# Optimization experiments

Hardware: AMD Instinct MI355X
Metric: run time of the kernel (lower is better)

Reference implementation:

```python
import jax, jax.numpy as jnp
import numpy as np

N, E, D, ED, SH = 100000, 1600000, 64, 16, 9

# Real spherical harmonics l=0,1,2, 'integral' normalization (e3nn default),
# applied to unit direction vectors. Coefficients: 1/(2*sqrt(pi)), sqrt(3/4pi), etc.

def _sh(d):
    x, y, z = d[:, 0], d[:, 1], d[:, 2]
    return jnp.stack([
        jnp.full_like(x, 0.28209479177387814),          # l=0
        0.4886025119029199 * y,                          # l=1, m=-1
        0.4886025119029199 * z,                          # l=1, m=0
        0.4886025119029199 * x,                          # l=1, m=1
        1.0925484305920792 * x * y,                      # l=2, m=-2
        1.0925484305920792 * y * z,                      # l=2, m=-1
        0.31539156525252005 * (3.0 * z * z - 1.0),       # l=2, m=0
        1.0925484305920792 * x * z,                      # l=2, m=1
        0.5462742152960396 * (x * x - y * y),            # l=2, m=2
    ], axis=1)


def _mlp(h, W1, b1, W2, b2):  # Linear -> SiLU -> Linear
    return jax.nn.silu(h @ W1 + b1) @ W2 + b2


def setup_inputs() -> dict:
    key = jax.random.key(0)
    ks = jax.random.split(key, 16)
    def rn(k, shape, scale=0.05):
        return jax.random.normal(k, shape, dtype=jnp.float32) * scale
    return {
        "x": jax.random.normal(ks[0], (N, D), jnp.float32),
        "pos": jax.random.normal(ks[1], (N, 3), jnp.float32) * 3.0,
        "edge_attr": jax.random.normal(ks[2], (E, ED), jnp.float32),
        "row": jax.random.randint(ks[3], (E,), 0, N, dtype=jnp.int32),
        "col": jax.random.randint(ks[4], (E,), 0, N, dtype=jnp.int32),
        "node_W1": rn(ks[5], (D, D)), "node_b1": jnp.zeros((D,), jnp.float32),
        "node_W2": rn(ks[6], (D, D)), "node_b2": jnp.zeros((D,), jnp.float32),
        "edge_W1": rn(ks[7], (SH + ED, D)), "edge_b1": jnp.zeros((D,), jnp.float32),
        "edge_W2": rn(ks[8], (D, D)), "edge_b2": jnp.zeros((D,), jnp.float32),
        "out_W1": rn(ks[9], (2 * D, D)), "out_b1": jnp.zeros((D,), jnp.float32),
        "out_W2": rn(ks[10], (D, D)), "out_b2": jnp.zeros((D,), jnp.float32),
        "bn_gamma": jnp.ones((D,), jnp.float32), "bn_beta": jnp.zeros((D,), jnp.float32),
    }


def reference(x, pos, edge_attr, row, col,
              node_W1, node_b1, node_W2, node_b2,
              edge_W1, edge_b1, edge_W2, edge_b2,
              out_W1, out_b1, out_W2, out_b2,
              bn_gamma, bn_beta):
    # gather node positions per edge -> relative vectors
    rel = pos[row] - pos[col]                                    # [E,3]
    length = jnp.sqrt(jnp.sum(rel * rel, axis=1, keepdims=True) + 1e-12)
    d = rel / length
    d = d / (jnp.sqrt(jnp.sum(d * d, axis=1, keepdims=True)) + 1e-10)
    edge_sh = _sh(d)                                             # [E,9]
    edge_feat = jnp.concatenate([edge_sh, edge_attr], axis=1)    # [E,9+ED]
    x_t = _mlp(x, node_W1, node_b1, node_W2, node_b2)            # [N,D]
    e_w = _mlp(edge_feat, edge_W1, edge_b1, edge_W2, edge_b2)    # [E,D]
    msg = x_t[row] * e_w                                         # message = x_j * edge_attr
    # scatter-mean onto target nodes (edge_index[1] == col)
    s = jax.ops.segment_sum(msg, col, num_segments=N)            # [N,D]
    cnt = jax.ops.segment_sum(jnp.ones((E,), msg.dtype), col, num_segments=N)
    agg = s / jnp.maximum(cnt, 1.0)[:, None]
    h = jnp.concatenate([agg, x], axis=1)                        # [N,2D]
    h = _mlp(h, out_W1, out_b1, out_W2, out_b2)                  # [N,D]
    # BatchNorm over node dim (scalar irreps), training-mode batch stats
    mean = jnp.mean(h, axis=0)
    var = jnp.var(h, axis=0)
    return (h - mean) / jnp.sqrt(var + 1e-5) * bn_gamma + bn_beta
```

## Files before the change

### kernel.cpp

```cpp
#include <hip/hip_runtime.h>
#include <math.h>

#define DD 64
#define EDA 16

#define FR_E1 0
#define FR_E2 4
#define FR_N1 12
#define FR_N2 20
#define FR_O1 28
#define FR_O2 44
#define FR_TOT 52

#define PADH 72
#define PADF 68

typedef unsigned int u32;
typedef __attribute__((ext_vector_type(8))) short short8;
typedef __attribute__((ext_vector_type(4))) float f32x4;

static __device__ __forceinline__ float silu(float v) {
    return v / (1.0f + __expf(-v));
}
static __device__ __forceinline__ unsigned short f2bf(float f) {
    unsigned u = __float_as_uint(f);
    unsigned r = u + 0x7FFFu + ((u >> 16) & 1u);
    return (unsigned short)(r >> 16);
}
static __device__ __forceinline__ float bf2f(unsigned short u) {
    return __uint_as_float(((unsigned)u) << 16);
}
static __device__ __forceinline__ unsigned cvt_pk_bf16(float lo, float hi) {
    unsigned r;
    asm("v_cvt_pk_bf16_f32 %0, %1, %2" : "=v"(r) : "v"(lo), "v"(hi));
    return r;
}

__global__ __launch_bounds__(256) void k_pack_w(
    const float* __restrict__ eW1, const float* __restrict__ eW2,
    const float* __restrict__ nW1, const float* __restrict__ nW2,
    const float* __restrict__ oW1, const float* __restrict__ oW2,
    unsigned short* __restrict__ wpk)
{
    int t = threadIdx.x;
    int nt = t >> 6, l = t & 63;
    int kc = l >> 4, n0 = l & 15;

    #pragma unroll
    for (int j = 0; j < 8; ++j) {
        int k = kc*8 + j;
        int orig = (k < 16) ? (9 + k) : ((k < 25) ? (k - 16) : -1);
        float v = (orig >= 0) ? eW1[orig*DD + nt*16 + n0] : 0.0f;
        wpk[((size_t)((FR_E1 + nt)*64 + l))*8 + j] = f2bf(v);
    }
    #pragma unroll
    for (int s = 0; s < 2; ++s) {
        #pragma unroll
        for (int j = 0; j < 8; ++j) {
            int k = s*32 + kc*8 + j;
            wpk[((size_t)((FR_E2 + s*4 + nt)*64 + l))*8 + j] = f2bf(eW2[k*DD + nt*16 + n0]);
            wpk[((size_t)((FR_N1 + s*4 + nt)*64 + l))*8 + j] = f2bf(nW1[k*DD + nt*16 + n0]);
            wpk[((size_t)((FR_N2 + s*4 + nt)*64 + l))*8 + j] = f2bf(nW2[k*DD + nt*16 + n0]);
            wpk[((size_t)((FR_O2 + s*4 + nt)*64 + l))*8 + j] = f2bf(oW2[k*DD + nt*16 + n0]);
        }
    }
    #pragma unroll
    for (int s = 0; s < 4; ++s) {
        #pragma unroll
        for (int j = 0; j < 8; ++j) {
            int k = s*32 + kc*8 + j;
            wpk[((size_t)((FR_O1 + s*4 + nt)*64 + l))*8 + j] = f2bf(oW1[k*DD + nt*16 + n0]);
        }
    }
}

__global__ __launch_bounds__(256) void k_hist(
    const int* __restrict__ col, u32* __restrict__ cnt, int n_e)
{
    int g = blockIdx.x * 256 + threadIdx.x;
    int base = g * 4;
    if (base + 3 < n_e) {
        int4 c = ((const int4*)col)[g];
        atomicAdd(&cnt[c.x], 1u);
        atomicAdd(&cnt[c.y], 1u);
        atomicAdd(&cnt[c.z], 1u);
        atomicAdd(&cnt[c.w], 1u);
    } else {
        for (int e = base; e < n_e; ++e) atomicAdd(&cnt[col[e]], 1u);
    }
}

__global__ __launch_bounds__(256) void k_scan1(
    const u32* __restrict__ cnt, u32* __restrict__ bsum, int n)
{
    __shared__ u32 s[256];
    int i = blockIdx.x * 256 + threadIdx.x;
    s[threadIdx.x] = (i < n) ? cnt[i] : 0u;
    __syncthreads();
    for (int o = 128; o > 0; o >>= 1) {
        if (threadIdx.x < o) s[threadIdx.x] += s[threadIdx.x + o];
        __syncthreads();
    }
    if (threadIdx.x == 0) bsum[blockIdx.x] = s[0];
}

__global__ __launch_bounds__(512) void k_scan2(
    const u32* __restrict__ bsum, u32* __restrict__ boff, int nb)
{
    __shared__ u32 s[512];
    int t = threadIdx.x;
    u32 v = (t < nb) ? bsum[t] : 0u;
    s[t] = v;
    __syncthreads();
    for (int o = 1; o < 512; o <<= 1) {
        u32 a = (t >= o) ? s[t - o] : 0u;
        __syncthreads();
        s[t] += a;
        __syncthreads();
    }
    if (t < nb) boff[t] = s[t] - v;
}

__global__ __launch_bounds__(256) void k_scan3(
    const u32* __restrict__ cnt, const u32* __restrict__ boff,
    u32* __restrict__ wp, int n)
{
    __shared__ u32 s[256];
    int t = threadIdx.x;
    int i = blockIdx.x * 256 + t;
    u32 v = (i < n) ? cnt[i] : 0u;
    s[t] = v;
    __syncthreads();
    for (int o = 1; o < 256; o <<= 1) {
        u32 a = (t >= o) ? s[t - o] : 0u;
        __syncthreads();
        s[t] += a;
        __syncthreads();
    }
    if (i < n) wp[i] = boff[blockIdx.x] + s[t] - v;
}

__global__ __launch_bounds__(256) void k_scatter(
    const int* __restrict__ row, const int* __restrict__ col,
    u32* __restrict__ wp,
    int* __restrict__ esorted, int* __restrict__ rsorted, int* __restrict__ csorted,
    int n_e)
{
    int e = blockIdx.x * 256 + threadIdx.x;
    if (e >= n_e) return;
    int c = col[e];
    u32 p = atomicAdd(&wp[c], 1u);
    esorted[p] = e;
    rsorted[p] = row[e];
    csorted[p] = c;
}

__global__ __launch_bounds__(256, 2) void k_node_mfma(
    const float* __restrict__ x,
    const unsigned short* __restrict__ wpk,
    const float* __restrict__ b1, const float* __restrict__ b2,
    unsigned short* __restrict__ x_tb, int n)
{
    __shared__ __align__(16) unsigned short tile[4][16*PADH];
    const int tid  = threadIdx.x;
    const int wv   = tid >> 6;
    const int lane = tid & 63;
    const int kc   = lane >> 4;
    const int n0   = lane & 15;
    const int rbase = kc * 4;

    const short8* fb = (const short8*)wpk;
    short8 bw1[2][4], bw2[2][4];
    #pragma unroll
    for (int s = 0; s < 2; ++s)
        #pragma unroll
        for (int nt = 0; nt < 4; ++nt) {
            bw1[s][nt] = fb[(FR_N1 + s*4 + nt)*64 + lane];
            bw2[s][nt] = fb[(FR_N2 + s*4 + nt)*64 + lane];
        }
    float b1v[4], b2v[4];
    #pragma unroll
    for (int nt = 0; nt < 4; ++nt) { b1v[nt] = b1[nt*16 + n0]; b2v[nt] = b2[nt*16 + n0]; }

    const int base = blockIdx.x*64 + wv*16;
    int rc = min(base + n0, n - 1);
    const float* xr = x + (size_t)rc * DD;

    short8 a[2];
    #pragma unroll
    for (int m = 0; m < 2; ++m) {
        float4 u0 = *(const float4*)(xr + m*32 + kc*8);
        float4 u1 = *(const float4*)(xr + m*32 + kc*8 + 4);
        unsigned* au = (unsigned*)&a[m];
        au[0] = cvt_pk_bf16(u0.x, u0.y);
        au[1] = cvt_pk_bf16(u0.z, u0.w);
        au[2] = cvt_pk_bf16(u1.x, u1.y);
        au[3] = cvt_pk_bf16(u1.z, u1.w);
    }

    f32x4 zz = {0.f, 0.f, 0.f, 0.f};
    f32x4 hacc[4] = {zz, zz, zz, zz};
    #pragma unroll
    for (int m = 0; m < 2; ++m)
        #pragma unroll
        for (int nt = 0; nt < 4; ++nt)
            hacc[nt] = __builtin_amdgcn_mfma_f32_16x16x32_bf16(a[m], bw1[m][nt], hacc[nt], 0, 0, 0);

    #pragma unroll
    for (int nt = 0; nt < 4; ++nt)
        #pragma unroll
        for (int r = 0; r < 4; ++r)
            tile[wv][(rbase + r)*PADH + nt*16 + n0] = f2bf(silu(hacc[nt][r] + b1v[nt]));
    __syncthreads();

    short8 a2_0 = *(const short8*)&tile[wv][n0*PADH +  0 + kc*8];
    short8 a2_1 = *(const short8*)&tile[wv][n0*PADH + 32 + kc*8];
    f32x4 oacc[4];
    #pragma unroll
    for (int nt = 0; nt < 4; ++nt) {
        oacc[nt] = __builtin_amdgcn_mfma_f32_16x16x32_bf16(a2_0, bw2[0][nt], zz, 0, 0, 0);
        oacc[nt] = __builtin_amdgcn_mfma_f32_16x16x32_bf16(a2_1, bw2[1][nt], oacc[nt], 0, 0, 0);
    }
    __syncthreads();

    #pragma unroll
    for (int nt = 0; nt < 4; ++nt)
        #pragma unroll
        for (int r = 0; r < 4; ++r)
            tile[wv][(rbase + r)*PADH + nt*16 + n0] = f2bf(oacc[nt][r] + b2v[nt]);
    __syncthreads();

    int ei = lane >> 2, q = lane & 3;
    int er = base + ei;
    if (er < n) {
        uint4* dst = (uint4*)(x_tb + (size_t)er * DD);
        dst[q]     = *(const uint4*)&tile[wv][ei*PADH + q*8];
        dst[q + 4] = *(const uint4*)&tile[wv][ei*PADH + (q + 4)*8];
    }
}

__global__ __launch_bounds__(256) void k_edge_fused(
    const float* __restrict__ pos,
    const float* __restrict__ edge_attr,
    const int* __restrict__ esorted, const int* __restrict__ rsorted,
    const int* __restrict__ csorted,
    const unsigned short* __restrict__ x_tb,
    const unsigned short* __restrict__ wpk,
    const float* __restrict__ b1, const float* __restrict__ b2,
    float* __restrict__ agg, int n_e)
{
    __shared__ __align__(16) unsigned short hid_s[4][16*PADH];
    __shared__ __align__(16) float          msg_s[4][16*PADF];
    __shared__ __align__(16) unsigned short xls[4][16*DD];
    __shared__ int col_s[4][64];

    const int tid  = threadIdx.x;
    const int wv   = tid >> 6;
    const int lane = tid & 63;
    const int kc   = lane >> 4;
    const int n0   = lane & 15;
    const int rb   = kc * 4;

    const short8* fb = (const short8*)wpk;
    short8 bw1[4], bw2[2][4];
    #pragma unroll
    for (int nt = 0; nt < 4; ++nt) bw1[nt] = fb[(FR_E1 + nt)*64 + lane];
    #pragma unroll
    for (int s = 0; s < 2; ++s)
        #pragma unroll
        for (int nt = 0; nt < 4; ++nt) bw2[s][nt] = fb[(FR_E2 + s*4 + nt)*64 + lane];

    float b1v[4], b2v[4];
    #pragma unroll
    for (int nt = 0; nt < 4; ++nt) { b1v[nt] = b1[nt*16 + n0]; b2v[nt] = b2[nt*16 + n0]; }

    const int gbase = blockIdx.x*256 + wv*64;
    int g  = gbase + lane;
    int gc = min(g, n_e - 1);
    int eo = esorted[gc];
    int rw = rsorted[gc];
    int cl = csorted[gc];
    col_s[wv][lane] = cl;

    float ax = pos[3*rw+0] - pos[3*cl+0];
    float ay = pos[3*rw+1] - pos[3*cl+1];
    float az = pos[3*rw+2] - pos[3*cl+2];
    float len = sqrtf(fmaf(ax,ax, fmaf(ay,ay, az*az)) + 1e-12f);
    float dx = ax/len, dy = ay/len, dz = az/len;
    float n2 = sqrtf(fmaf(dx,dx, fmaf(dy,dy, dz*dz)));
    float inv = 1.0f/(n2 + 1e-10f);
    dx *= inv; dy *= inv; dz *= inv;

    float sh[9];
    sh[0] = 0.28209479177387814f;
    sh[1] = 0.4886025119029199f*dy;
    sh[2] = 0.4886025119029199f*dz;
    sh[3] = 0.4886025119029199f*dx;
    sh[4] = 1.0925484305920792f*dx*dy;
    sh[5] = 1.0925484305920792f*dy*dz;
    sh[6] = 0.31539156525252005f*(3.0f*dz*dz - 1.0f);
    sh[7] = 1.0925484305920792f*dx*dz;
    sh[8] = 0.5462742152960396f*(dx*dx - dy*dy);

    f32x4 zz = {0.f, 0.f, 0.f, 0.f};

    #pragma unroll 1
    for (int t = 0; t < 4; ++t) {
        {
            int lr = t*16 + (lane >> 2);
            int rv = __shfl(rw, lr);
            int ch = lane & 3;
            const uint4* src = (const uint4*)(x_tb + (size_t)rv * DD);
            uint4 v0 = src[ch*2], v1 = src[ch*2 + 1];
            uint4* d = (uint4*)&xls[wv][(lr - t*16)*DD];
            d[ch*2]     = v0;
            d[ch*2 + 1] = v1;
        }

        int le = t*16 + n0;
        float shv[8], sh8;
        #pragma unroll
        for (int j = 0; j < 8; ++j) shv[j] = __shfl(sh[j], le);
        sh8 = __shfl(sh[8], le);

        float fv[8];
        #pragma unroll
        for (int j = 0; j < 8; ++j) fv[j] = 0.0f;
        if (kc < 2) {
            int ea = __shfl(eo, le);
            const float4* ap = (const float4*)(edge_attr + (size_t)ea*EDA + kc*8);
            float4 a0 = ap[0], a1 = ap[1];
            fv[0]=a0.x; fv[1]=a0.y; fv[2]=a0.z; fv[3]=a0.w;
            fv[4]=a1.x; fv[5]=a1.y; fv[6]=a1.z; fv[7]=a1.w;
        } else if (kc == 2) {
            #pragma unroll
            for (int j = 0; j < 8; ++j) fv[j] = shv[j];
        } else {
            fv[0] = sh8;
        }

        short8 af;
        {
            unsigned* au = (unsigned*)&af;
            au[0] = cvt_pk_bf16(fv[0], fv[1]);
            au[1] = cvt_pk_bf16(fv[2], fv[3]);
            au[2] = cvt_pk_bf16(fv[4], fv[5]);
            au[3] = cvt_pk_bf16(fv[6], fv[7]);
        }

        f32x4 hacc[4];
        #pragma unroll
        for (int nt = 0; nt < 4; ++nt)
            hacc[nt] = __builtin_amdgcn_mfma_f32_16x16x32_bf16(af, bw1[nt], zz, 0, 0, 0);

        #pragma unroll
        for (int nt = 0; nt < 4; ++nt)
            #pragma unroll
            for (int r = 0; r < 4; ++r)
                hid_s[wv][(rb + r)*PADH + nt*16 + n0] = f2bf(silu(hacc[nt][r] + b1v[nt]));
        __syncthreads();

        short8 a2_0 = *(const short8*)&hid_s[wv][n0*PADH +  0 + kc*8];
        short8 a2_1 = *(const short8*)&hid_s[wv][n0*PADH + 32 + kc*8];
        f32x4 oacc[4];
        #pragma unroll
        for (int nt = 0; nt < 4; ++nt) {
            oacc[nt] = __builtin_amdgcn_mfma_f32_16x16x32_bf16(a2_0, bw2[0][nt], zz, 0, 0, 0);
            oacc[nt] = __builtin_amdgcn_mfma_f32_16x16x32_bf16(a2_1, bw2[1][nt], oacc[nt], 0, 0, 0);
        }

        #pragma unroll
        for (int r = 0; r < 4; ++r) {
            int lrow = rb + r;
            bool rv2 = (gbase + t*16 + lrow) < n_e;
            #pragma unroll
            for (int nt = 0; nt < 4; ++nt) {
                float xv = bf2f(xls[wv][lrow*DD + nt*16 + n0]);
                float m  = (oacc[nt][r] + b2v[nt]) * xv;
                msg_s[wv][lrow*PADF + nt*16 + n0] = rv2 ? m : 0.0f;
            }
        }
        __syncthreads();

        {
            const int* cs = &col_s[wv][t*16];
            float acc = 0.0f;
            #pragma unroll
            for (int r = 0; r < 16; ++r) {
                acc += msg_s[wv][r*PADF + lane];
                int cur = cs[r];
                bool flush = (r == 15) || (cs[r+1] != cur);
                if (flush) {
                    unsafeAtomicAdd(&agg[(size_t)cur*DD + lane], acc);
                    acc = 0.0f;
                }
            }
        }
        __syncthreads();
    }
}

__global__ __launch_bounds__(256, 2) void k_out_mfma(
    const float* __restrict__ agg, const u32* __restrict__ cnt,
    const float* __restrict__ x,
    const unsigned short* __restrict__ wpk,
    const float* __restrict__ b1, const float* __restrict__ b2,
    float* __restrict__ h, float* __restrict__ sums, int n)
{
    __shared__ __align__(16) unsigned short htile[4][16*PADH];
    __shared__ __align__(16) float otile[4][16*PADF];
    const int tid  = threadIdx.x;
    const int wv   = tid >> 6;
    const int lane = tid & 63;
    const int kc   = lane >> 4;
    const int n0   = lane & 15;
    const int rbase = kc * 4;

    const short8* fb = (const short8*)wpk;
    short8 bw1[4][4], bw2[2][4];
    #pragma unroll
    for (int s = 0; s < 4; ++s)
        #pragma unroll
        for (int nt = 0; nt < 4; ++nt) bw1[s][nt] = fb[(FR_O1 + s*4 + nt)*64 + lane];
    #pragma unroll
    for (int s = 0; s < 2; ++s)
        #pragma unroll
        for (int nt = 0; nt < 4; ++nt) bw2[s][nt] = fb[(FR_O2 + s*4 + nt)*64 + lane];

    float b1v[4], b2v[4];
    #pragma unroll
    for (int nt = 0; nt < 4; ++nt) { b1v[nt] = b1[nt*16 + n0]; b2v[nt] = b2[nt*16 + n0]; }

    const int base = blockIdx.x*64 + wv*16;
    int rc = min(base + n0, n - 1);
    const float* ar = agg + (size_t)rc * DD;
    const float* xr = x   + (size_t)rc * DD;
    float invc = 1.0f / fmaxf((float)cnt[rc], 1.0f);

    short8 a[4];
    #pragma unroll
    for (int m = 0; m < 4; ++m) {
        const float* src = (m < 2) ? (ar + m*32 + kc*8) : (xr + (m-2)*32 + kc*8);
        float4 u0 = *(const float4*)(src);
        float4 u1 = *(const float4*)(src + 4);
        if (m < 2) {
            u0.x*=invc; u0.y*=invc; u0.z*=invc; u0.w*=invc;
            u1.x*=invc; u1.y*=invc; u1.z*=invc; u1.w*=invc;
        }
        unsigned* au = (unsigned*)&a[m];
        au[0] = cvt_pk_bf16(u0.x, u0.y);
        au[1] = cvt_pk_bf16(u0.z, u0.w);
        au[2] = cvt_pk_bf16(u1.x, u1.y);
        au[3] = cvt_pk_bf16(u1.z, u1.w);
    }

    f32x4 zz = {0.f, 0.f, 0.f, 0.f};
    f32x4 hacc[4] = {zz, zz, zz, zz};
    #pragma unroll
    for (int m = 0; m < 4; ++m)
        #pragma unroll
        for (int nt = 0; nt < 4; ++nt)
            hacc[nt] = __builtin_amdgcn_mfma_f32_16x16x32_bf16(a[m], bw1[m][nt], hacc[nt], 0, 0, 0);

    #pragma unroll
    for (int nt = 0; nt < 4; ++nt)
        #pragma unroll
        for (int r = 0; r < 4; ++r)
            htile[wv][(rbase + r)*PADH + nt*16 + n0] = f2bf(silu(hacc[nt][r] + b1v[nt]));
    __syncthreads();

    short8 a2_0 = *(const short8*)&htile[wv][n0*PADH +  0 + kc*8];
    short8 a2_1 = *(const short8*)&htile[wv][n0*PADH + 32 + kc*8];
    f32x4 oacc[4];
    #pragma unroll
    for (int nt = 0; nt < 4; ++nt) {
        oacc[nt] = __builtin_amdgcn_mfma_f32_16x16x32_bf16(a2_0, bw2[0][nt], zz, 0, 0, 0);
        oacc[nt] = __builtin_amdgcn_mfma_f32_16x16x32_bf16(a2_1, bw2[1][nt], oacc[nt], 0, 0, 0);
    }

    #pragma unroll
    for (int nt = 0; nt < 4; ++nt)
        #pragma unroll
        for (int r = 0; r < 4; ++r)
            otile[wv][(rbase + r)*PADF + nt*16 + n0] = oacc[nt][r] + b2v[nt];
    __syncthreads();

    int ei = lane >> 2, q = lane & 3;
    int er = base + ei;
    if (er < n) {
        float4* dst = (float4*)(h + (size_t)er * DD);
        #pragma unroll
        for (int k = 0; k < 4; ++k)
            dst[q + 4*k] = *(const float4*)&otile[wv][ei*PADF + (q + 4*k)*4];
    }

    if (tid < 64) {
        int f = tid;
        float s = 0.f, qq = 0.f;
        #pragma unroll
        for (int w = 0; w < 4; ++w) {
            int base_w = blockIdx.x*64 + w*16;
            int nv = n - base_w;
            nv = nv < 0 ? 0 : (nv > 16 ? 16 : nv);
            for (int r = 0; r < nv; ++r) {
                float v = otile[w][r*PADF + f];
                s += v; qq = fmaf(v, v, qq);
            }
        }
        unsafeAtomicAdd(&sums[f], s);
        unsafeAtomicAdd(&sums[DD + f], qq);
    }
}

__global__ void k_bn_finalize(const float* __restrict__ sums,
                              const float* __restrict__ gamma, const float* __restrict__ beta,
                              float* __restrict__ ss, float inv_n)
{
    int j = threadIdx.x;
    float m = sums[j] * inv_n;
    float var = sums[DD+j] * inv_n - m*m;
    float sc = gamma[j] * rsqrtf(var + 1e-5f);
    ss[j] = sc;
    ss[DD+j] = beta[j] - m*sc;
}

__global__ __launch_bounds__(256) void k_bn_norm(
    float* __restrict__ h, const float* __restrict__ ss, int total4)
{
    int g = blockIdx.x*256 + threadIdx.x;
    if (g >= total4) return;
    int f0 = (g*4) & (DD-1);
    float4 v = ((const float4*)h)[g];
    v.x = fmaf(v.x, ss[f0+0], ss[DD+f0+0]);
    v.y = fmaf(v.y, ss[f0+1], ss[DD+f0+1]);
    v.z = fmaf(v.z, ss[f0+2], ss[DD+f0+2]);
    v.w = fmaf(v.w, ss[f0+3], ss[DD+f0+3]);
    ((float4*)h)[g] = v;
}

static inline size_t al16(size_t v) { return (v + 15) & ~(size_t)15; }

extern "C" void kernel_launch(void* const* d_in, const int* in_sizes, int n_in,
                              void* d_out, int out_size, void* d_ws, size_t ws_size,
                              hipStream_t stream)
{
    const float* x         = (const float*)d_in[0];
    const float* pos       = (const float*)d_in[1];
    const float* edge_attr = (const float*)d_in[2];
    const int*   row       = (const int*)d_in[3];
    const int*   col       = (const int*)d_in[4];
    const float* nW1 = (const float*)d_in[5];
    const float* nb1 = (const float*)d_in[6];
    const float* nW2 = (const float*)d_in[7];
    const float* nb2 = (const float*)d_in[8];
    const float* eW1 = (const float*)d_in[9];
    const float* eb1 = (const float*)d_in[10];
    const float* eW2 = (const float*)d_in[11];
    const float* eb2 = (const float*)d_in[12];
    const float* oW1 = (const float*)d_in[13];
    const float* ob1 = (const float*)d_in[14];
    const float* oW2 = (const float*)d_in[15];
    const float* ob2 = (const float*)d_in[16];
    const float* gamma = (const float*)d_in[17];
    const float* beta  = (const float*)d_in[18];

    const int N = in_sizes[0] / DD;
    const int E = in_sizes[3];
    const int NB = (N + 255) / 256;

    float* hout = (float*)d_out;
    char* ws = (char*)d_ws;

    size_t o_xtb  = 0;
    size_t o_cnt  = o_xtb  + (size_t)N*DD*2;
    size_t o_sums = o_cnt  + (size_t)N*4;
    size_t o_agg  = o_sums + 128*4;
    size_t o_ss   = o_agg  + (size_t)N*DD*4;
    size_t o_wp   = o_ss   + 128*4;
    size_t o_bsum = o_wp   + (size_t)N*4;
    size_t o_boff = al16(o_bsum + (size_t)NB*4);
    size_t o_wpk  = al16(o_boff + (size_t)NB*4);
    size_t o_eso  = al16(o_wpk + (size_t)FR_TOT*64*8*2);
    size_t o_rso  = o_eso + (size_t)E*4;
    size_t o_cso  = o_rso + (size_t)E*4;
    size_t need   = o_cso + (size_t)E*4;

    if (ws_size < need) return;

    unsigned short* x_tb = (unsigned short*)(ws + o_xtb);
    u32*   cnt  = (u32*)(ws + o_cnt);
    float* sums = (float*)(ws + o_sums);
    float* agg  = (float*)(ws + o_agg);
    float* ssb  = (float*)(ws + o_ss);
    u32*   wp   = (u32*)(ws + o_wp);
    u32*   bsum = (u32*)(ws + o_bsum);
    u32*   boff = (u32*)(ws + o_boff);
    unsigned short* wpk = (unsigned short*)(ws + o_wpk);
    int* esorted = (int*)(ws + o_eso);
    int* rsorted = (int*)(ws + o_rso);
    int* csorted = (int*)(ws + o_cso);

    hipMemsetAsync(cnt, 0, (size_t)N*4 + 128*4 + (size_t)N*DD*4, stream);

    k_pack_w<<<1, 256, 0, stream>>>(eW1, eW2, nW1, nW2, oW1, oW2, wpk);
    k_hist <<<(E/4 + 255)/256, 256, 0, stream>>>(col, cnt, E);
    k_scan1<<<NB, 256, 0, stream>>>(cnt, bsum, N);
    k_scan2<<<1, 512, 0, stream>>>(bsum, boff, NB);
    k_scan3<<<NB, 256, 0, stream>>>(cnt, boff, wp, N);
    k_scatter<<<(E + 255)/256, 256, 0, stream>>>(row, col, wp, esorted, rsorted, csorted, E);
    k_node_mfma<<<(N + 63)/64, 256, 0, stream>>>(x, wpk, nb1, nb2, x_tb, N);
    k_edge_fused<<<(E + 255)/256, 256, 0, stream>>>(pos, edge_attr, esorted, rsorted, csorted,
                                                    x_tb, wpk, eb1, eb2, agg, E);
    k_out_mfma<<<(N + 63)/64, 256, 0, stream>>>(agg, cnt, x, wpk, ob1, ob2, hout, sums, N);
    k_bn_finalize<<<1, 64, 0, stream>>>(sums, gamma, beta, ssb, 1.0f/(float)N);
    k_bn_norm<<<(N*DD/4 + 255)/256, 256, 0, stream>>>(hout, ssb, N*DD/4);
}
```

Before: 359.1 us.

## Pack sorted edge indices into 64-bit words and use wave-local LDS fences

The three separate sorted index arrays (edge id, row, col) become one 8-byte packed record per edge (21-bit edge id, 17-bit row, 26-bit col). This cuts index traffic in the scatter and edge kernels. The edge kernel replaces block-wide __syncthreads with per-wave lgkmcnt waits, since each wave owns its own LDS slices. It also swaps the MFMA operand order so each lane produces contiguous output columns, enabling vectorized LDS stores. Spherical harmonics are staged through LDS as bf16 instead of being passed by shuffles, and occupancy is raised to 3 blocks per CU. The packing assumes the edge count stays below 2^21 and the node count below 2^17, and the wave-local fences rely on no cross-wave LDS sharing.

```diff
diff --git a/kernel.cpp b/kernel.cpp
--- a/kernel.cpp
+++ b/kernel.cpp
@@ -15,6 +15,10 @@
 #define PADH 72
 #define PADF 68
 
+#define HS 72
+#define XS 72
+#define PF 68
+
 typedef unsigned int u32;
 typedef __attribute__((ext_vector_type(8))) short short8;
 typedef __attribute__((ext_vector_type(4))) float f32x4;
@@ -34,6 +38,10 @@
     unsigned r;
     asm("v_cvt_pk_bf16_f32 %0, %1, %2" : "=v"(r) : "v"(lo), "v"(hi));
     return r;
+}
+static __device__ __forceinline__ void wave_lds_fence() {
+    asm volatile("s_waitcnt lgkmcnt(0)" ::: "memory");
+    __builtin_amdgcn_sched_barrier(0);
 }
 
 __global__ __launch_bounds__(256) void k_pack_w(
@@ -142,17 +150,17 @@
 
 __global__ __launch_bounds__(256) void k_scatter(
     const int* __restrict__ row, const int* __restrict__ col,
-    u32* __restrict__ wp,
-    int* __restrict__ esorted, int* __restrict__ rsorted, int* __restrict__ csorted,
-    int n_e)
+    u32* __restrict__ wp, uint2* __restrict__ ce, int n_e)
 {
     int e = blockIdx.x * 256 + threadIdx.x;
     if (e >= n_e) return;
     int c = col[e];
+    int r = row[e];
     u32 p = atomicAdd(&wp[c], 1u);
-    esorted[p] = e;
-    rsorted[p] = row[e];
-    csorted[p] = c;
+    uint2 pk;
+    pk.x = (u32)e | ((u32)r << 21);
+    pk.y = ((u32)r >> 11) | ((u32)c << 6);
+    ce[p] = pk;
 }
 
 __global__ __launch_bounds__(256, 2) void k_node_mfma(
@@ -239,27 +247,26 @@
     }
 }
 
-__global__ __launch_bounds__(256) void k_edge_fused(
+__global__ __launch_bounds__(256, 3) void k_edge_fused(
     const float* __restrict__ pos,
     const float* __restrict__ edge_attr,
-    const int* __restrict__ esorted, const int* __restrict__ rsorted,
-    const int* __restrict__ csorted,
+    const uint2* __restrict__ ce,
     const unsigned short* __restrict__ x_tb,
     const unsigned short* __restrict__ wpk,
     const float* __restrict__ b1, const float* __restrict__ b2,
     float* __restrict__ agg, int n_e)
 {
-    __shared__ __align__(16) unsigned short hid_s[4][16*PADH];
-    __shared__ __align__(16) float          msg_s[4][16*PADF];
-    __shared__ __align__(16) unsigned short xls[4][16*DD];
-    __shared__ int col_s[4][64];
+    __shared__ __align__(16) unsigned short hid_s[4][16*HS];
+    __shared__ __align__(16) float          msg_s[4][16*PF];
+    __shared__ __align__(16) unsigned short xls[4][16*XS];
+    __shared__ __align__(16) u32            sh_s[4][64*8];
+    __shared__ int r_s[4][64], c_s[4][64], e_s[4][64];
 
     const int tid  = threadIdx.x;
     const int wv   = tid >> 6;
     const int lane = tid & 63;
     const int kc   = lane >> 4;
     const int n0   = lane & 15;
-    const int rb   = kc * 4;
 
     const short8* fb = (const short8*)wpk;
     short8 bw1[4], bw2[2][4];
@@ -270,17 +277,21 @@
         #pragma unroll
         for (int nt = 0; nt < 4; ++nt) bw2[s][nt] = fb[(FR_E2 + s*4 + nt)*64 + lane];
 
-    float b1v[4], b2v[4];
-    #pragma unroll
-    for (int nt = 0; nt < 4; ++nt) { b1v[nt] = b1[nt*16 + n0]; b2v[nt] = b2[nt*16 + n0]; }
+    float4 b1q[4], b2q[4];
+    #pragma unroll
+    for (int nt = 0; nt < 4; ++nt) {
+        b1q[nt] = *(const float4*)(b1 + nt*16 + kc*4);
+        b2q[nt] = *(const float4*)(b2 + nt*16 + kc*4);
+    }
 
     const int gbase = blockIdx.x*256 + wv*64;
     int g  = gbase + lane;
     int gc = min(g, n_e - 1);
-    int eo = esorted[gc];
-    int rw = rsorted[gc];
-    int cl = csorted[gc];
-    col_s[wv][lane] = cl;
+    uint2 pk = ce[gc];
+    int eo = pk.x & 0x1FFFFF;
+    int rw = (pk.x >> 21) | ((pk.y & 0x3Fu) << 11);
+    int cl = (int)(pk.y >> 6);
+    r_s[wv][lane] = rw; c_s[wv][lane] = cl; e_s[wv][lane] = eo;
 
     float ax = pos[3*rw+0] - pos[3*cl+0];
     float ay = pos[3*rw+1] - pos[3*cl+1];
@@ -291,112 +302,120 @@
     float inv = 1.0f/(n2 + 1e-10f);
     dx *= inv; dy *= inv; dz *= inv;
 
-    float sh[9];
-    sh[0] = 0.28209479177387814f;
-    sh[1] = 0.4886025119029199f*dy;
-    sh[2] = 0.4886025119029199f*dz;
-    sh[3] = 0.4886025119029199f*dx;
-    sh[4] = 1.0925484305920792f*dx*dy;
-    sh[5] = 1.0925484305920792f*dy*dz;
-    sh[6] = 0.31539156525252005f*(3.0f*dz*dz - 1.0f);
-    sh[7] = 1.0925484305920792f*dx*dz;
-    sh[8] = 0.5462742152960396f*(dx*dx - dy*dy);
+    float sh0 = 0.28209479177387814f;
+    float sh1 = 0.4886025119029199f*dy;
+    float sh2 = 0.4886025119029199f*dz;
+    float sh3 = 0.4886025119029199f*dx;
+    float sh4 = 1.0925484305920792f*dx*dy;
+    float sh5 = 1.0925484305920792f*dy*dz;
+    float sh6 = 0.31539156525252005f*(3.0f*dz*dz - 1.0f);
+    float sh7 = 1.0925484305920792f*dx*dz;
+    float sh8 = 0.5462742152960396f*(dx*dx - dy*dy);
+
+    {
+        uint4 sp;
+        sp.x = cvt_pk_bf16(sh0, sh1);
+        sp.y = cvt_pk_bf16(sh2, sh3);
+        sp.z = cvt_pk_bf16(sh4, sh5);
+        sp.w = cvt_pk_bf16(sh6, sh7);
+        u32* d = &sh_s[wv][lane*8];
+        *(uint4*)d = sp;
+        d[4] = cvt_pk_bf16(sh8, 0.0f);
+    }
 
     f32x4 zz = {0.f, 0.f, 0.f, 0.f};
 
     #pragma unroll 1
     for (int t = 0; t < 4; ++t) {
+        wave_lds_fence();
+
         {
-            int lr = t*16 + (lane >> 2);
-            int rv = __shfl(rw, lr);
-            int ch = lane & 3;
-            const uint4* src = (const uint4*)(x_tb + (size_t)rv * DD);
+            int lr = lane >> 2, ch = lane & 3;
+            int rrow = r_s[wv][t*16 + lr];
+            bool v = (gbase + t*16 + lr) < n_e;
+            const uint4* src = (const uint4*)(x_tb + (size_t)rrow * DD);
             uint4 v0 = src[ch*2], v1 = src[ch*2 + 1];
-            uint4* d = (uint4*)&xls[wv][(lr - t*16)*DD];
-            d[ch*2]     = v0;
-            d[ch*2 + 1] = v1;
-        }
-
-        int le = t*16 + n0;
-        float shv[8], sh8;
-        #pragma unroll
-        for (int j = 0; j < 8; ++j) shv[j] = __shfl(sh[j], le);
-        sh8 = __shfl(sh[8], le);
-
-        float fv[8];
-        #pragma unroll
-        for (int j = 0; j < 8; ++j) fv[j] = 0.0f;
+            if (!v) { v0 = make_uint4(0,0,0,0); v1 = make_uint4(0,0,0,0); }
+            *(uint4*)&xls[wv][lr*XS + ch*16]     = v0;
+            *(uint4*)&xls[wv][lr*XS + ch*16 + 8] = v1;
+        }
+
+        short8 af;
+        unsigned* au = (unsigned*)&af;
         if (kc < 2) {
-            int ea = __shfl(eo, le);
+            int ea = e_s[wv][t*16 + n0];
             const float4* ap = (const float4*)(edge_attr + (size_t)ea*EDA + kc*8);
             float4 a0 = ap[0], a1 = ap[1];
-            fv[0]=a0.x; fv[1]=a0.y; fv[2]=a0.z; fv[3]=a0.w;
-            fv[4]=a1.x; fv[5]=a1.y; fv[6]=a1.z; fv[7]=a1.w;
+            au[0] = cvt_pk_bf16(a0.x, a0.y);
+            au[1] = cvt_pk_bf16(a0.z, a0.w);
+            au[2] = cvt_pk_bf16(a1.x, a1.y);
+            au[3] = cvt_pk_bf16(a1.z, a1.w);
         } else if (kc == 2) {
-            #pragma unroll
-            for (int j = 0; j < 8; ++j) fv[j] = shv[j];
+            uint4 s4 = *(const uint4*)&sh_s[wv][(t*16 + n0)*8];
+            au[0] = s4.x; au[1] = s4.y; au[2] = s4.z; au[3] = s4.w;
         } else {
-            fv[0] = sh8;
-        }
-
-        short8 af;
+            au[0] = sh_s[wv][(t*16 + n0)*8 + 4];
+            au[1] = 0; au[2] = 0; au[3] = 0;
+        }
+
+        f32x4 hacc[4];
+        #pragma unroll
+        for (int nt = 0; nt < 4; ++nt)
+            hacc[nt] = __builtin_amdgcn_mfma_f32_16x16x32_bf16(bw1[nt], af, zz, 0, 0, 0);
+
+        #pragma unroll
+        for (int nt = 0; nt < 4; ++nt) {
+            float h0 = silu(hacc[nt][0] + b1q[nt].x);
+            float h1 = silu(hacc[nt][1] + b1q[nt].y);
+            float h2 = silu(hacc[nt][2] + b1q[nt].z);
+            float h3 = silu(hacc[nt][3] + b1q[nt].w);
+            uint2 pr;
+            pr.x = cvt_pk_bf16(h0, h1);
+            pr.y = cvt_pk_bf16(h2, h3);
+            *(uint2*)&hid_s[wv][n0*HS + nt*16 + kc*4] = pr;
+        }
+        wave_lds_fence();
+
+        short8 bf0 = *(const short8*)&hid_s[wv][n0*HS +  0 + kc*8];
+        short8 bf1 = *(const short8*)&hid_s[wv][n0*HS + 32 + kc*8];
+        f32x4 oacc[4];
+        #pragma unroll
+        for (int nt = 0; nt < 4; ++nt) {
+            oacc[nt] = __builtin_amdgcn_mfma_f32_16x16x32_bf16(bw2[0][nt], bf0, zz, 0, 0, 0);
+            oacc[nt] = __builtin_amdgcn_mfma_f32_16x16x32_bf16(bw2[1][nt], bf1, oacc[nt], 0, 0, 0);
+        }
+
+        #pragma unroll
+        for (int nt = 0; nt < 4; ++nt) {
+            uint2 xv = *(const uint2*)&xls[wv][n0*XS + nt*16 + kc*4];
+            float x0 = bf2f((unsigned short)(xv.x));
+            float x1 = bf2f((unsigned short)(xv.x >> 16));
+            float x2 = bf2f((unsigned short)(xv.y));
+            float x3 = bf2f((unsigned short)(xv.y >> 16));
+            float4 m;
+            m.x = (oacc[nt][0] + b2q[nt].x) * x0;
+            m.y = (oacc[nt][1] + b2q[nt].y) * x1;
+            m.z = (oacc[nt][2] + b2q[nt].z) * x2;
+            m.w = (oacc[nt][3] + b2q[nt].w) * x3;
+            *(float4*)&msg_s[wv][n0*PF + nt*16 + kc*4] = m;
+        }
+        wave_lds_fence();
+
         {
-            unsigned* au = (unsigned*)&af;
-            au[0] = cvt_pk_bf16(fv[0], fv[1]);
-            au[1] = cvt_pk_bf16(fv[2], fv[3]);
-            au[2] = cvt_pk_bf16(fv[4], fv[5]);
-            au[3] = cvt_pk_bf16(fv[6], fv[7]);
-        }
-
-        f32x4 hacc[4];
-        #pragma unroll
-        for (int nt = 0; nt < 4; ++nt)
-            hacc[nt] = __builtin_amdgcn_mfma_f32_16x16x32_bf16(af, bw1[nt], zz, 0, 0, 0);
-
-        #pragma unroll
-        for (int nt = 0; nt < 4; ++nt)
-            #pragma unroll
-            for (int r = 0; r < 4; ++r)
-                hid_s[wv][(rb + r)*PADH + nt*16 + n0] = f2bf(silu(hacc[nt][r] + b1v[nt]));
-        __syncthreads();
-
-        short8 a2_0 = *(const short8*)&hid_s[wv][n0*PADH +  0 + kc*8];
-        short8 a2_1 = *(const short8*)&hid_s[wv][n0*PADH + 32 + kc*8];
-        f32x4 oacc[4];
-        #pragma unroll
-        for (int nt = 0; nt < 4; ++nt) {
-            oacc[nt] = __builtin_amdgcn_mfma_f32_16x16x32_bf16(a2_0, bw2[0][nt], zz, 0, 0, 0);
-            oacc[nt] = __builtin_amdgcn_mfma_f32_16x16x32_bf16(a2_1, bw2[1][nt], oacc[nt], 0, 0, 0);
-        }
-
-        #pragma unroll
-        for (int r = 0; r < 4; ++r) {
-            int lrow = rb + r;
-            bool rv2 = (gbase + t*16 + lrow) < n_e;
-            #pragma unroll
-            for (int nt = 0; nt < 4; ++nt) {
-                float xv = bf2f(xls[wv][lrow*DD + nt*16 + n0]);
-                float m  = (oacc[nt][r] + b2v[nt]) * xv;
-                msg_s[wv][lrow*PADF + nt*16 + n0] = rv2 ? m : 0.0f;
-            }
-        }
-        __syncthreads();
-
-        {
-            const int* cs = &col_s[wv][t*16];
+            const int* cs = &c_s[wv][t*16];
             float acc = 0.0f;
             #pragma unroll
             for (int r = 0; r < 16; ++r) {
-                acc += msg_s[wv][r*PADF + lane];
+                acc += msg_s[wv][r*PF + lane];
                 int cur = cs[r];
-                bool flush = (r == 15) || (cs[r+1] != cur);
-                if (flush) {
+                if (r == 15) {
+                    unsafeAtomicAdd(&agg[(size_t)cur*DD + lane], acc);
+                } else if (cs[r+1] != cur) {
                     unsafeAtomicAdd(&agg[(size_t)cur*DD + lane], acc);
                     acc = 0.0f;
                 }
             }
         }
-        __syncthreads();
     }
 }
 
@@ -580,10 +599,8 @@
     size_t o_bsum = o_wp   + (size_t)N*4;
     size_t o_boff = al16(o_bsum + (size_t)NB*4);
     size_t o_wpk  = al16(o_boff + (size_t)NB*4);
-    size_t o_eso  = al16(o_wpk + (size_t)FR_TOT*64*8*2);
-    size_t o_rso  = o_eso + (size_t)E*4;
-    size_t o_cso  = o_rso + (size_t)E*4;
-    size_t need   = o_cso + (size_t)E*4;
+    size_t o_ce   = al16(o_wpk + (size_t)FR_TOT*64*8*2);
+    size_t need   = o_ce + (size_t)E*8;
 
     if (ws_size < need) return;
 
@@ -596,9 +613,7 @@
     u32*   bsum = (u32*)(ws + o_bsum);
     u32*   boff = (u32*)(ws + o_boff);
     unsigned short* wpk = (unsigned short*)(ws + o_wpk);
-    int* esorted = (int*)(ws + o_eso);
-    int* rsorted = (int*)(ws + o_rso);
-    int* csorted = (int*)(ws + o_cso);
+    uint2* ce   = (uint2*)(ws + o_ce);
 
     hipMemsetAsync(cnt, 0, (size_t)N*4 + 128*4 + (size_t)N*DD*4, stream);
 
@@ -607,10 +622,10 @@
     k_scan1<<<NB, 256, 0, stream>>>(cnt, bsum, N);
     k_scan2<<<1, 512, 0, stream>>>(bsum, boff, NB);
     k_scan3<<<NB, 256, 0, stream>>>(cnt, boff, wp, N);
-    k_scatter<<<(E + 255)/256, 256, 0, stream>>>(row, col, wp, esorted, rsorted, csorted, E);
+    k_scatter<<<(E + 255)/256, 256, 0, stream>>>(row, col, wp, ce, E);
     k_node_mfma<<<(N + 63)/64, 256, 0, stream>>>(x, wpk, nb1, nb2, x_tb, N);
-    k_edge_fused<<<(E + 255)/256, 256, 0, stream>>>(pos, edge_attr, esorted, rsorted, csorted,
-                                                    x_tb, wpk, eb1, eb2, agg, E);
+    k_edge_fused<<<(E + 255)/256, 256, 0, stream>>>(pos, edge_attr, ce, x_tb,
+                                                    wpk, eb1, eb2, agg, E);
     k_out_mfma<<<(N + 63)/64, 256, 0, stream>>>(agg, cnt, x, wpk, ob1, ob2, hout, sums, N);
     k_bn_finalize<<<1, 64, 0, stream>>>(sums, gamma, beta, ssb, 1.0f/(float)N);
     k_bn_norm<<<(N*DD/4 + 255)/256, 256, 0, stream>>>(hout, ssb, N*DD/4);
```

After: 414.3 us. 15.4% more time.
